# Optimization experiments

Measured on AMD Instinct MI355X. Metric: run time of the kernel, lower is better.

The kernel has to match this reference:

```python
import jax, jax.numpy as jnp
import numpy as np

# LightGCN propagation constants
N_USERS = 50000
N_ITEMS = 100000
N_NODES = N_USERS + N_ITEMS          # rows of the symmetric normalized adjacency
N_EDGES = 2400000                    # nnz of sparse adjacency (avg degree ~16)
LATENT_DIM = 64                      # config['latent_dim_rec']
N_LAYERS = 3                         # config['lightGCN_n_layers']
BATCH = 4096


def setup_inputs() -> dict:
    key = jax.random.key(0)
    ks = jax.random.split(key, 7)
    # Embedding tables, init std=0.1 as in nn.init.normal_(std=0.1)
    emb_user = 0.1 * jax.random.normal(ks[0], (N_USERS, LATENT_DIM), dtype=jnp.float32)
    emb_item = 0.1 * jax.random.normal(ks[1], (N_ITEMS, LATENT_DIM), dtype=jnp.float32)
    # Sparse normalized adjacency in COO form (fixed structure reused every layer)
    src = jax.random.randint(ks[2], (N_EDGES,), 0, N_NODES, dtype=jnp.int32)
    dst = jax.random.randint(ks[3], (N_EDGES,), 0, N_NODES, dtype=jnp.int32)
    # values ~ 1/sqrt(deg_i * deg_j) scale for avg degree 16
    vals = jax.random.uniform(ks[4], (N_EDGES,), dtype=jnp.float32) / 16.0
    users = jax.random.randint(ks[5], (BATCH,), 0, N_USERS, dtype=jnp.int32)
    items = jax.random.randint(ks[6], (BATCH,), 0, N_ITEMS, dtype=jnp.int32)
    return {"emb_user": emb_user, "emb_item": emb_item, "vals": vals,
            "src": src, "dst": dst, "users": users, "items": items}


def _spmm(vals, src, dst, x):
    # y[dst] += vals * x[src]  == torch.sparse.mm(G, x)
    return jax.ops.segment_sum(vals[:, None] * x[src], dst, num_segments=N_NODES)


def reference(emb_user, emb_item, vals, src, dst, users, items):
    # computer(): stack layer embeddings and mean-pool, fused as running sum
    all_emb = jnp.concatenate([emb_user, emb_item], axis=0)  # [N, D]
    acc = all_emb
    x = all_emb
    for _ in range(N_LAYERS):
        x = _spmm(vals, src, dst, x)
        acc = acc + x
    light_out = acc / jnp.asarray(N_LAYERS + 1, dtype=acc.dtype)
    users_emb = light_out[users]                 # [B, D]
    items_emb = light_out[N_USERS + items]       # [B, D]
    gamma = jnp.sum(users_emb * items_emb, axis=1)  # [B]
    return gamma
```

## Files before the change

### kernel.cpp

```cpp
#include <hip/hip_runtime.h>


#define N_USERS 50000
#define N_ITEMS 100000
#define N_NODES 150000
#define N_EDGES 2400000
#define DIM 64
#define BATCH 4096

#define CHUNKS 256
#define CHUNK_EDGES 9375
#define PPT 10
#define KB 256
#define NPB 586
#define ECAP 10240
#define CONVB 2344

typedef unsigned int uint;
typedef float v2f __attribute__((ext_vector_type(2)));

__device__ __forceinline__ uint pack_bf16(float a, float b) {
    uint ua = __float_as_uint(a), ub = __float_as_uint(b);
    ua = (ua + 0x7FFFu + ((ua >> 16) & 1u)) >> 16;
    ub = (ub + 0x7FFFu + ((ub >> 16) & 1u)) >> 16;
    return ua | (ub << 16);
}

__device__ __forceinline__ v2f unpack_bf16x2(uint w) {
    v2f r;
    r.x = __uint_as_float(w << 16);
    r.y = __uint_as_float(w & 0xFFFF0000u);
    return r;
}

__global__ __launch_bounds__(1024) void part_kernel(
        const int* __restrict__ src, const int* __restrict__ dstA,
        const float* __restrict__ vals, int* __restrict__ gcur,
        int2* __restrict__ coarse,
        const float* __restrict__ emb_user, const float* __restrict__ emb_item,
        uint2* __restrict__ t0) {
    int t = threadIdx.x;
    if (blockIdx.x >= CHUNKS) {
        int i = (blockIdx.x - CHUNKS) * 1024 + t;
        if (i < N_NODES * DIM / 4) {
            const int userN4 = N_USERS * DIM / 4;
            float4 v;
            if (i < userN4) v = ((const float4*)emb_user)[i];
            else            v = ((const float4*)emb_item)[i - userN4];
            t0[i] = make_uint2(pack_bf16(v.x, v.y), pack_bf16(v.z, v.w));
        }
        return;
    }
    __shared__ int h[KB];
    __shared__ int cur[KB];
    int c = blockIdx.x;
    if (t < KB) h[t] = 0;
    __syncthreads();
    int base = c * CHUNK_EDGES;
    int d_c[PPT];
#pragma unroll
    for (int u = 0; u < PPT; ++u) {
        int i = t + u * 1024;
        d_c[u] = 0;
        if (i < CHUNK_EDGES) {
            int d = dstA[base + i];
            d_c[u] = d;
            atomicAdd(&h[(int)((unsigned)d / NPB)], 1);
        }
    }
    __syncthreads();
    if (t < KB) cur[t] = atomicAdd(&gcur[t], h[t]);
    __syncthreads();
#pragma unroll
    for (int u = 0; u < PPT; ++u) {
        int i = t + u * 1024;
        if (i < CHUNK_EDGES) {
            int e = base + i;
            int d = d_c[u];
            int b = (int)((unsigned)d / NPB);
            int dl = d - b * NPB;
            int p = atomicAdd(&cur[b], 1);
            if (p < ECAP)
                coarse[b * ECAP + p] = make_int2(src[e] | (dl << 18),
                                                 __float_as_int(vals[e]));
        }
    }
}

__global__ __launch_bounds__(1024) void p4f_fine(int2* __restrict__ coarse,
                                                 const int* __restrict__ gcur,
                                                 uint* __restrict__ rowinfo) {
    __shared__ int2 eds[ECAP];
    __shared__ int cnt[640];
    __shared__ int rs_[640];
    __shared__ int cur_[640];
    __shared__ int wsum[16];
    int k = blockIdx.x, t = threadIdx.x;
    int rbase = k * ECAP;
    int ne = min(gcur[k], ECAP);
    for (int i = t; i < ne; i += 1024) eds[i] = coarse[rbase + i];
    if (t < 640) cnt[t] = 0;
    __syncthreads();
    for (int i = t; i < ne; i += 1024)
        atomicAdd(&cnt[eds[i].x >> 18], 1);
    __syncthreads();
    int wid = t >> 6, lane = t & 63;
    if (t < 640) {
        int v = cnt[t];
        int incl = v;
#pragma unroll
        for (int o = 1; o < 64; o <<= 1) {
            int add = __shfl_up(incl, o, 64);
            if (lane >= o) incl += add;
        }
        rs_[t] = incl - v;
        if (lane == 63) wsum[wid] = incl;
    }
    __syncthreads();
    if (t < 64) {
        int vv = (lane < 10) ? wsum[lane] : 0;
        int inc2 = vv;
#pragma unroll
        for (int o = 1; o < 16; o <<= 1) {
            int add = __shfl_up(inc2, o, 64);
            if (lane >= o) inc2 += add;
        }
        if (lane < 10) wsum[lane] = inc2 - vv;
    }
    __syncthreads();
    if (t < 640) rs_[t] += wsum[wid];
    __syncthreads();
    int nodes0 = k * NPB;
    int nb = min(NPB, N_NODES - nodes0);
    if (t < nb)
        rowinfo[nodes0 + t] = (uint)(rbase + rs_[t]) | ((uint)cnt[t] << 22);
    if (t < 640) cur_[t] = rs_[t];
    __syncthreads();
    for (int i = t; i < ne; i += 1024) {
        int2 ev = eds[i];
        int dl = ev.x >> 18;
        int p = atomicAdd(&cur_[dl], 1);
        coarse[rbase + p] = make_int2(ev.x & 0x3FFFF, ev.y);
    }
}

__global__ __launch_bounds__(256) void spmm_kernel(
        const uint* __restrict__ rowinfo, const int2* __restrict__ epair,
        const uint* __restrict__ xin, uint* __restrict__ xout) {
    int wave = (blockIdx.x * 256 + threadIdx.x) >> 6;
    int lane = threadIdx.x & 63;
    int g = lane >> 3;
    int l = lane & 7;
    int n = wave * 8 + g;
    bool live = n < N_NODES;
    uint ri = live ? rowinfo[n] : 0u;
    int s = (int)(ri & 0x3FFFFFu);
    int e = live ? s + (int)(ri >> 22) : s;
    int gbase = g * 8;
    v2f a0 = {0.f, 0.f}, a1 = {0.f, 0.f}, a2 = {0.f, 0.f}, a3 = {0.f, 0.f};
    for (int jb = s; jb < e; jb += 8) {
        int jl = jb + l;
        int2 ev = epair[jl < e ? jl : (e - 1)];
        float vw = (jl < e) ? __int_as_float(ev.y) : 0.f;
        int sx = ev.x;
        int srcs[8];
        float ws[8];
#pragma unroll
        for (int u = 0; u < 8; ++u) {
            srcs[u] = __shfl(sx, gbase + u, 64);
            ws[u]   = __shfl(vw, gbase + u, 64);
        }
        uint4 r[8];
#pragma unroll
        for (int u = 0; u < 8; ++u)
            r[u] = ((const uint4*)(xin + (size_t)srcs[u] * 32))[l];
#pragma unroll
        for (int u = 0; u < 8; ++u) {
            a0 += ws[u] * unpack_bf16x2(r[u].x);
            a1 += ws[u] * unpack_bf16x2(r[u].y);
            a2 += ws[u] * unpack_bf16x2(r[u].z);
            a3 += ws[u] * unpack_bf16x2(r[u].w);
        }
    }
    if (live) {
        uint4 o;
        o.x = pack_bf16(a0.x, a0.y);
        o.y = pack_bf16(a1.x, a1.y);
        o.z = pack_bf16(a2.x, a2.y);
        o.w = pack_bf16(a3.x, a3.y);
        ((uint4*)(xout + (size_t)n * 32))[l] = o;
    }
}

__global__ __launch_bounds__(256) void batch_row_kernel(
        const int* __restrict__ users, const int* __restrict__ items,
        const float* __restrict__ emb_user, const float* __restrict__ emb_item,
        const uint* __restrict__ x1, const uint* __restrict__ x2,
        const uint* __restrict__ rowinfo, const int2* __restrict__ epair,
        float4* __restrict__ rows) {
    int w = (blockIdx.x * 256 + threadIdx.x) >> 6;
    int lane = threadIdx.x & 63;
    int g = lane >> 4;
    int l = lane & 15;
    bool isU = w < BATCH;
    int b = isU ? w : w - BATCH;
    int idx = isU ? users[b] : items[b];
    int n = isU ? idx : N_USERS + idx;
    uint ri = rowinfo[n];
    int s = (int)(ri & 0x3FFFFFu);
    int e = s + (int)(ri >> 22);
    v2f a0 = {0.f, 0.f}, a1 = {0.f, 0.f};
    for (int j0 = s + g; j0 < e; j0 += 16) {
        int2 ev[4];
        float vv[4];
        uint2 rr[4];
#pragma unroll
        for (int u = 0; u < 4; ++u) {
            int j = j0 + 4 * u;
            bool p = (u == 0) || (j < e);
            ev[u] = epair[p ? j : j0];
            vv[u] = p ? __int_as_float(ev[u].y) : 0.f;
        }
#pragma unroll
        for (int u = 0; u < 4; ++u)
            rr[u] = ((const uint2*)(x2 + (size_t)ev[u].x * 32))[l];
#pragma unroll
        for (int u = 0; u < 4; ++u) {
            a0 += vv[u] * unpack_bf16x2(rr[u].x);
            a1 += vv[u] * unpack_bf16x2(rr[u].y);
        }
    }
#pragma unroll
    for (int off = 16; off < 64; off <<= 1) {
        a0.x += __shfl_xor(a0.x, off, 64);
        a0.y += __shfl_xor(a0.y, off, 64);
        a1.x += __shfl_xor(a1.x, off, 64);
        a1.y += __shfl_xor(a1.y, off, 64);
    }
    if (g == 0) {
        const float* t0row = isU ? (emb_user + (size_t)idx * DIM)
                                 : (emb_item + (size_t)idx * DIM);
        float4 x0 = ((const float4*)t0row)[l];
        uint2 w1 = ((const uint2*)(x1 + (size_t)n * 32))[l];
        uint2 w2 = ((const uint2*)(x2 + (size_t)n * 32))[l];
        v2f b10 = unpack_bf16x2(w1.x), b11 = unpack_bf16x2(w1.y);
        v2f b20 = unpack_bf16x2(w2.x), b21 = unpack_bf16x2(w2.y);
        float4 r;
        r.x = x0.x + b10.x + b20.x + a0.x;
        r.y = x0.y + b10.y + b20.y + a0.y;
        r.z = x0.z + b11.x + b21.x + a1.x;
        r.w = x0.w + b11.y + b21.y + a1.y;
        rows[(size_t)w * 16 + l] = r;
    }
}

__global__ __launch_bounds__(256) void dot_kernel(const float* __restrict__ rows,
                                                  float* __restrict__ out) {
    int t = blockIdx.x * 256 + threadIdx.x;
    int b = t >> 6;
    int lane = t & 63;
    float p = rows[(size_t)b * DIM + lane] * rows[(size_t)(BATCH + b) * DIM + lane];
#pragma unroll
    for (int o = 32; o > 0; o >>= 1) p += __shfl_down(p, o, 64);
    if (lane == 0) out[b] = p * (1.0f / 16.0f);
}

extern "C" void kernel_launch(void* const* d_in, const int* in_sizes, int n_in,
                              void* d_out, int out_size, void* d_ws, size_t ws_size,
                              hipStream_t stream) {
    const float* emb_user = (const float*)d_in[0];
    const float* emb_item = (const float*)d_in[1];
    const float* vals     = (const float*)d_in[2];
    const int*   src      = (const int*)d_in[3];
    const int*   dst      = (const int*)d_in[4];
    const int*   users    = (const int*)d_in[5];
    const int*   items    = (const int*)d_in[6];
    float* out = (float*)d_out;

    char* ws = (char*)d_ws;
    size_t off = 0;
    auto walloc = [&](size_t bytes) -> void* {
        void* p = ws + off;
        off += (bytes + 255) & ~(size_t)255;
        return p;
    };
    const size_t ROWB = (size_t)N_NODES * DIM * 2;
    uint* t0          = (uint*)walloc(ROWB);
    uint* x1          = (uint*)walloc(ROWB);
    uint* x2          = (uint*)walloc(ROWB);
    int2* coarse      = (int2*)walloc((size_t)KB * ECAP * 8);
    int*  gcur        = (int*) walloc((size_t)KB * 4);
    uint* rowinfo     = (uint*)walloc((size_t)N_NODES * 4);
    float4* rows      = (float4*)walloc((size_t)2 * BATCH * DIM * 4);

    hipMemsetAsync(gcur, 0, (size_t)KB * 4, stream);

    part_kernel<<<CHUNKS + CONVB, 1024, 0, stream>>>(
        src, dst, vals, gcur, coarse, emb_user, emb_item, (uint2*)t0);
    p4f_fine<<<KB, 1024, 0, stream>>>(coarse, gcur, rowinfo);

    const int SPMM_BLOCKS = (N_NODES / 8 * 64 + 255) / 256;
    spmm_kernel<<<SPMM_BLOCKS, 256, 0, stream>>>(rowinfo, coarse, t0, x1);
    spmm_kernel<<<SPMM_BLOCKS, 256, 0, stream>>>(rowinfo, coarse, x1, x2);
    batch_row_kernel<<<(2 * BATCH) / 4, 256, 0, stream>>>(
        users, items, emb_user, emb_item, x1, x2, rowinfo, coarse, rows);
    dot_kernel<<<(BATCH * 64) / 256, 256, 0, stream>>>((const float*)rows, out);
}
```

Before: 256.1 us.

## Stage partitioned edges in shared memory for coalesced bucket writes

```diff
diff --git a/kernel.cpp b/kernel.cpp
--- a/kernel.cpp
+++ b/kernel.cpp
@@ -14,6 +14,7 @@
 #define KB 256
 #define NPB 586
 #define ECAP 10240
+#define GSTR 16
 #define CONVB 2344
 
 typedef unsigned int uint;
@@ -51,25 +52,60 @@
         }
         return;
     }
+    __shared__ int2 stage[CHUNK_EDGES];
+    __shared__ unsigned char stage_b[CHUNK_EDGES];
     __shared__ int h[KB];
-    __shared__ int cur[KB];
+    __shared__ int hoff[KB];
+    __shared__ int delta[KB];
+    __shared__ int wsum4[4];
     int c = blockIdx.x;
     if (t < KB) h[t] = 0;
     __syncthreads();
     int base = c * CHUNK_EDGES;
     int d_c[PPT];
+    int r_c[PPT];
 #pragma unroll
     for (int u = 0; u < PPT; ++u) {
         int i = t + u * 1024;
         d_c[u] = 0;
+        r_c[u] = 0;
         if (i < CHUNK_EDGES) {
             int d = dstA[base + i];
             d_c[u] = d;
-            atomicAdd(&h[(int)((unsigned)d / NPB)], 1);
-        }
-    }
-    __syncthreads();
-    if (t < KB) cur[t] = atomicAdd(&gcur[t], h[t]);
+            r_c[u] = atomicAdd(&h[(int)((unsigned)d / NPB)], 1);
+        }
+    }
+    __syncthreads();
+    int lane = t & 63, wid = t >> 6;
+    if (t < KB) {
+        int v = h[t];
+        int incl = v;
+#pragma unroll
+        for (int o = 1; o < 64; o <<= 1) {
+            int add = __shfl_up(incl, o, 64);
+            if (lane >= o) incl += add;
+        }
+        hoff[t] = incl - v;
+        if (lane == 63) wsum4[wid] = incl;
+    }
+    __syncthreads();
+    if (t < 64) {
+        int vv = (lane < 4) ? wsum4[lane] : 0;
+        int inc2 = vv;
+#pragma unroll
+        for (int o = 1; o < 4; o <<= 1) {
+            int add = __shfl_up(inc2, o, 64);
+            if (lane >= o) inc2 += add;
+        }
+        if (lane < 4) wsum4[lane] = inc2 - vv;
+    }
+    __syncthreads();
+    if (t < KB) {
+        int off = hoff[t] + wsum4[t >> 6];
+        hoff[t] = off;
+        int cb = atomicAdd(&gcur[t * GSTR], h[t]);
+        delta[t] = t * ECAP + cb - off;
+    }
     __syncthreads();
 #pragma unroll
     for (int u = 0; u < PPT; ++u) {
@@ -79,10 +115,20 @@
             int d = d_c[u];
             int b = (int)((unsigned)d / NPB);
             int dl = d - b * NPB;
-            int p = atomicAdd(&cur[b], 1);
-            if (p < ECAP)
-                coarse[b * ECAP + p] = make_int2(src[e] | (dl << 18),
-                                                 __float_as_int(vals[e]));
+            int pos = hoff[b] + r_c[u];
+            stage[pos] = make_int2(src[e] | (dl << 18), __float_as_int(vals[e]));
+            stage_b[pos] = (unsigned char)b;
+        }
+    }
+    __syncthreads();
+#pragma unroll
+    for (int u = 0; u < PPT; ++u) {
+        int j = t + u * 1024;
+        if (j < CHUNK_EDGES) {
+            int b = stage_b[j];
+            int idx = j + delta[b];
+            if (idx < (b + 1) * ECAP)
+                coarse[idx] = stage[j];
         }
     }
 }
@@ -97,7 +143,7 @@
     __shared__ int wsum[16];
     int k = blockIdx.x, t = threadIdx.x;
     int rbase = k * ECAP;
-    int ne = min(gcur[k], ECAP);
+    int ne = min(gcur[k * GSTR], ECAP);
     for (int i = t; i < ne; i += 1024) eds[i] = coarse[rbase + i];
     if (t < 640) cnt[t] = 0;
     __syncthreads();
@@ -289,11 +335,11 @@
     uint* x1          = (uint*)walloc(ROWB);
     uint* x2          = (uint*)walloc(ROWB);
     int2* coarse      = (int2*)walloc((size_t)KB * ECAP * 8);
-    int*  gcur        = (int*) walloc((size_t)KB * 4);
+    int*  gcur        = (int*) walloc((size_t)KB * GSTR * 4);
     uint* rowinfo     = (uint*)walloc((size_t)N_NODES * 4);
     float4* rows      = (float4*)walloc((size_t)2 * BATCH * DIM * 4);
 
-    hipMemsetAsync(gcur, 0, (size_t)KB * 4, stream);
+    hipMemsetAsync(gcur, 0, (size_t)KB * GSTR * 4, stream);
 
     part_kernel<<<CHUNKS + CONVB, 1024, 0, stream>>>(
         src, dst, vals, gcur, coarse, emb_user, emb_item, (uint2*)t0);
```

Measured after the change: 244.0 us. 4.7% less time.
